# Optimization experiments

Measured on AMD Instinct MI355X. Metric: run time of the kernel, lower is better.

Reference implementation:

```python
import jax, jax.numpy as jnp
import numpy as np

N, E = 50000, 400000
IN, HID, LAT = 64, 64, 64


def _lin(key, fi, fo):
    return jax.random.normal(key, (fi, fo), jnp.float32) / np.sqrt(fi)


def setup_inputs() -> dict:
    key = jax.random.key(0)
    ks = jax.random.split(key, 24)
    inp = {
        'x': jax.random.normal(ks[0], (N, IN), jnp.float32),
        'edge_index': jax.random.randint(ks[1], (2, E), 0, N, dtype=jnp.int32),
        'batch': jnp.zeros((N,), jnp.int32),
    }
    # conv1: heads=1, out=HID, no residual
    inp.update(Wl1=_lin(ks[2], IN, HID), bl1=jnp.zeros(HID), Wr1=_lin(ks[3], IN, HID), br1=jnp.zeros(HID),
               att1=jax.random.normal(ks[4], (1, HID)) / np.sqrt(HID), bo1=jnp.zeros(HID))
    # conv2: heads=4, out=2*HID//4 per head (concat -> 2*HID), residual
    O2 = 2 * HID // 4
    inp.update(Wl2=_lin(ks[5], HID, 4 * O2), bl2=jnp.zeros(4 * O2), Wr2=_lin(ks[6], HID, 4 * O2), br2=jnp.zeros(4 * O2),
               att2=jax.random.normal(ks[7], (4, O2)) / np.sqrt(O2), bo2=jnp.zeros(4 * O2), Wres2=_lin(ks[8], HID, 4 * O2))
    # conv3: heads=4, out=HID per head (concat -> 4*HID), residual
    O3 = HID
    inp.update(Wl3=_lin(ks[9], 2 * HID, 4 * O3), bl3=jnp.zeros(4 * O3), Wr3=_lin(ks[10], 2 * HID, 4 * O3), br3=jnp.zeros(4 * O3),
               att3=jax.random.normal(ks[11], (4, O3)) / np.sqrt(O3), bo3=jnp.zeros(4 * O3), Wres3=_lin(ks[12], 2 * HID, 4 * O3))
    inp.update(ln1_g=jnp.ones(HID), ln1_b=jnp.zeros(HID), ln2_g=jnp.ones(2 * HID), ln2_b=jnp.zeros(2 * HID),
               ln3_g=jnp.ones(4 * HID), ln3_b=jnp.zeros(4 * HID))
    inp.update(enc_W=_lin(ks[13], 4 * HID, LAT), enc_b=jnp.zeros(LAT), rp_W=_lin(ks[14], IN, LAT), rp_b=jnp.zeros(LAT))
    inp.update(d1_W=_lin(ks[15], LAT, 2 * HID), d1_b=jnp.zeros(2 * HID), d2_W=_lin(ks[16], 2 * HID, HID), d2_b=jnp.zeros(HID),
               d3_W=_lin(ks[17], HID, IN), d3_b=jnp.zeros(IN))
    return inp


def _gatv2(x, src, tgt, Wl, bl, Wr, br, att, bo, heads, oc, Wres=None):
    # GATv2: e_ij = att . leaky_relu(Wr x_i + Wl x_j), softmax over in-neighbors of i,
    # out_i = sum_j alpha_ij * (Wl x_j); concat heads; optional linear residual.
    n = x.shape[0]
    xl = (x @ Wl + bl).reshape(n, heads, oc)  # source transform
    xr = (x @ Wr + br).reshape(n, heads, oc)  # target transform
    xj = xl[src]                              # [E, H, C] gathered source feats
    e = jnp.einsum('ehc,hc->eh', jax.nn.leaky_relu(xr[tgt] + xj, 0.2), att)
    m = jax.ops.segment_max(e, tgt, num_segments=n)          # stable segment softmax
    p = jnp.exp(e - m[tgt])
    alpha = p / jax.ops.segment_sum(p, tgt, num_segments=n)[tgt]
    out = jax.ops.segment_sum(alpha[:, :, None] * xj, tgt, num_segments=n).reshape(n, heads * oc)
    if Wres is not None:
        out = out + x @ Wres
    return out + bo


def _gnorm(x, g, b):
    # PyG LayerNorm(mode='graph') with batch=None: normalize over ALL nodes and features
    mu = jnp.mean(x)
    d = x - mu
    var = jnp.mean(d * d)
    return d * jax.lax.rsqrt(var + 1e-5) * g + b


def reference(x, edge_index, batch, Wl1, bl1, Wr1, br1, att1, bo1,
              Wl2, bl2, Wr2, br2, att2, bo2, Wres2,
              Wl3, bl3, Wr3, br3, att3, bo3, Wres3,
              ln1_g, ln1_b, ln2_g, ln2_b, ln3_g, ln3_b,
              enc_W, enc_b, rp_W, rp_b, d1_W, d1_b, d2_W, d2_b, d3_W, d3_b):
    n = x.shape[0]
    loop = jnp.arange(n, dtype=edge_index.dtype)  # add_self_loops=True (GATv2Conv default)
    src = jnp.concatenate([edge_index[0], loop])
    tgt = jnp.concatenate([edge_index[1], loop])
    h1 = jax.nn.relu(_gnorm(_gatv2(x, src, tgt, Wl1, bl1, Wr1, br1, att1, bo1, 1, HID), ln1_g, ln1_b))
    h2 = jax.nn.relu(_gnorm(_gatv2(h1, src, tgt, Wl2, bl2, Wr2, br2, att2, bo2, 4, 2 * HID // 4, Wres2), ln2_g, ln2_b))
    h3 = jax.nn.relu(_gnorm(_gatv2(h2, src, tgt, Wl3, bl3, Wr3, br3, att3, bo3, 4, HID, Wres3), ln3_g, ln3_b))
    z_nodes = jax.nn.relu(h3 @ enc_W + enc_b) + (x @ rp_W + rp_b)  # dropout inactive (eval)
    ones = jnp.ones((n, 1), z_nodes.dtype)
    z_graph = jax.ops.segment_sum(z_nodes, batch, num_segments=1) / jax.ops.segment_sum(ones, batch, num_segments=1)
    h = jax.nn.relu(z_nodes @ d1_W + d1_b)
    h = jax.nn.relu(h @ d2_W + d2_b)
    x_hat = h @ d3_W + d3_b
    return (z_nodes, x_hat, z_graph)
```

## Files before the change

### kernel.cpp

```cpp
#include <hip/hip_runtime.h>
#include <math.h>

typedef __attribute__((ext_vector_type(8))) short short8;
typedef __attribute__((ext_vector_type(4))) float f32x4;
typedef _Float16 h2 __attribute__((ext_vector_type(2)));

__device__ __forceinline__ unsigned short f2bf(float f) {
  union { float f; unsigned u; } c; c.f = f;
  unsigned r = c.u + 0x7fffu + ((c.u >> 16) & 1u);
  return (unsigned short)(r >> 16);
}
__device__ __forceinline__ float bf2f(unsigned short u) {
  union { unsigned u; float f; } c; c.u = ((unsigned)u) << 16;
  return c.f;
}
__device__ __forceinline__ void dot2(float& e, h2 a, h2 b) {
  asm("v_dot2_f32_f16 %0, %1, %2, %0" : "+v"(e) : "v"(a), "v"(b));
}

__global__ void zero_k(int* __restrict__ deg, int n, float* __restrict__ stats,
                       float* __restrict__ zg) {
  int i = blockIdx.x * 256 + threadIdx.x;
  if (i < n) deg[i] = 0;
  if (i < 768) stats[i] = 0.f;
  if (i < 64) zg[i] = 0.f;
}

__global__ void hist_k(const int* __restrict__ tgt, int* __restrict__ deg, int E) {
  int stride = gridDim.x * blockDim.x;
  for (int e = blockIdx.x * blockDim.x + threadIdx.x; e < E; e += stride)
    atomicAdd(&deg[tgt[e]], 1);
}

__global__ void scan1_k(const int* __restrict__ deg, int* __restrict__ bsum, int n) {
  __shared__ int sh[256];
  int idx = blockIdx.x * 256 + threadIdx.x;
  sh[threadIdx.x] = (idx < n) ? deg[idx] : 0;
  __syncthreads();
  for (int off = 128; off > 0; off >>= 1) {
    if (threadIdx.x < off) sh[threadIdx.x] += sh[threadIdx.x + off];
    __syncthreads();
  }
  if (threadIdx.x == 0) bsum[blockIdx.x] = sh[0];
}

__global__ void scan2_k(int* __restrict__ bsum, int nb) {
  __shared__ int sh[256];
  int t = threadIdx.x;
  int v = (t < nb) ? bsum[t] : 0;
  sh[t] = v; __syncthreads();
  for (int off = 1; off < 256; off <<= 1) {
    int add = (t >= off) ? sh[t - off] : 0;
    __syncthreads();
    sh[t] += add;
    __syncthreads();
  }
  if (t < nb) bsum[t] = sh[t] - v;
}

__global__ void scan3_k(const int* __restrict__ deg, const int* __restrict__ bsum,
                        int* __restrict__ starts, int* __restrict__ cursor, int n) {
  __shared__ int sh[256];
  int t = threadIdx.x;
  int idx = blockIdx.x * 256 + t;
  int v = (idx < n) ? deg[idx] : 0;
  sh[t] = v; __syncthreads();
  for (int off = 1; off < 256; off <<= 1) {
    int add = (t >= off) ? sh[t - off] : 0;
    __syncthreads();
    sh[t] += add;
    __syncthreads();
  }
  if (idx < n) {
    int ex = bsum[blockIdx.x] + sh[t] - v;
    starts[idx] = ex;
    cursor[idx] = ex;
  }
}

__global__ void scatter_k(const int* __restrict__ src, const int* __restrict__ tgt,
                          int* __restrict__ cursor, int* __restrict__ esrc, int E) {
  int stride = gridDim.x * blockDim.x;
  for (int e = blockIdx.x * blockDim.x + threadIdx.x; e < E; e += stride) {
    int p = atomicAdd(&cursor[tgt[e]], 1);
    esrc[p] = src[e];
  }
}

__global__ void cvt_k(const float* __restrict__ src, unsigned short* __restrict__ dst,
                      size_t n4) {
  size_t stride = (size_t)gridDim.x * blockDim.x;
  for (size_t i = (size_t)blockIdx.x * blockDim.x + threadIdx.x; i < n4; i += stride) {
    float4 v = reinterpret_cast<const float4*>(src)[i];
    ushort4 o;
    o.x = f2bf(v.x); o.y = f2bf(v.y); o.z = f2bf(v.z); o.w = f2bf(v.w);
    reinterpret_cast<ushort4*>(dst)[i] = o;
  }
}

struct WSeg { const float* W; unsigned short* T; int K; int F; int base; };
struct WPack { WSeg s[13]; int total; };
__global__ __launch_bounds__(256) void wconv_all_k(WPack p) {
  int idx = blockIdx.x * 256 + threadIdx.x;
  if (idx >= p.total) return;
  int si = 0;
#pragma unroll
  for (int i = 1; i < 13; ++i) si = (idx >= p.s[i].base) ? i : si;
  const WSeg sg = p.s[si];
  const int loc = idx - sg.base;
  const int k = loc / sg.F, f = loc - k * sg.F;
  sg.T[(size_t)f * sg.K + k] = f2bf(sg.W[loc]);
}

template <int K, int F, int SETS, int LNF, int OM0, int ACT1>
__global__ __launch_bounds__(256) void mg_k(
    const unsigned short* __restrict__ X, const float* __restrict__ bins,
    const float* __restrict__ lng, const float* __restrict__ lnb, float invNF,
    const unsigned short* __restrict__ WT0, const float* __restrict__ B0,
    const unsigned short* __restrict__ WT1, const float* __restrict__ B1,
    const unsigned short* __restrict__ WT2,
    _Float16* __restrict__ Y0, _Float16* __restrict__ Y1,
    unsigned short* __restrict__ Y2b, float* __restrict__ Y2f, int n) {
  constexpr int NK = K / 32;
  constexpr int TL = F / 64;
  constexpr int CPR = K / 8;
  __shared__ unsigned short As[64 * K];
  __shared__ float lnp[2];
  char* asb = (char*)As;
  const int tid = threadIdx.x;
  const int lane = tid & 63;
  const int wv = tid >> 6;
  const int r0 = blockIdx.x * 64;

  if (LNF) {
    if (tid < 64) {
      float s1 = bins[tid] + bins[tid + 64];
      float s2 = bins[tid + 128] + bins[tid + 192];
#pragma unroll
      for (int mm = 1; mm < 64; mm <<= 1) {
        s1 += __shfl_xor(s1, mm, 64);
        s2 += __shfl_xor(s2, mm, 64);
      }
      if (tid == 0) {
        const float mu = s1 * invNF;
        lnp[0] = mu;
        lnp[1] = rsqrtf(s2 * invNF - mu * mu + 1e-5f);
      }
    }
    __syncthreads();
  }
  const float mu = LNF ? lnp[0] : 0.f;
  const float rs = LNF ? lnp[1] : 0.f;

  for (int c = tid; c < 64 * CPR; c += 256) {
    const int row = c / CPR;
    const int k0 = (c - row * CPR) * 8;
    const int gr = r0 + row;
    short8 a = {0, 0, 0, 0, 0, 0, 0, 0};
    if (gr < n) {
      a = *reinterpret_cast<const short8*>(&X[(size_t)gr * K + k0]);
      if (LNF) {
        float g[8], bb[8];
        *(float4*)&g[0] = *(const float4*)&lng[k0];
        *(float4*)&g[4] = *(const float4*)&lng[k0 + 4];
        *(float4*)&bb[0] = *(const float4*)&lnb[k0];
        *(float4*)&bb[4] = *(const float4*)&lnb[k0 + 4];
#pragma unroll
        for (int q = 0; q < 8; ++q) {
          float f = bf2f((unsigned short)a[q]);
          f = fmaxf(fmaf(f - mu, rs * g[q], bb[q]), 0.f);
          a[q] = (short)f2bf(f);
        }
      }
    }
    const int boff = ((row * K + k0) * 2) ^ ((row & 7) << 4);
    *(short8*)(asb + boff) = a;
  }
  __syncthreads();

  const int rl = lane & 15;
  const int ks = lane >> 4;
#pragma unroll
  for (int set = 0; set < SETS; ++set) {
    const unsigned short* WT = (set == 0) ? WT0 : (set == 1) ? WT1 : WT2;
    f32x4 acc[4][TL];
#pragma unroll
    for (int rt = 0; rt < 4; ++rt)
#pragma unroll
      for (int t = 0; t < TL; ++t) acc[rt][t] = (f32x4){0.f, 0.f, 0.f, 0.f};
#pragma unroll
    for (int kk = 0; kk < NK; ++kk) {
      short8 bf[TL];
#pragma unroll
      for (int t = 0; t < TL; ++t)
        bf[t] = *reinterpret_cast<const short8*>(
            &WT[(size_t)((wv * TL + t) * 16 + rl) * K + kk * 32 + ks * 8]);
      short8 af[4];
#pragma unroll
      for (int rt = 0; rt < 4; ++rt) {
        const int row = rt * 16 + rl;
        const int boff = ((row * K + kk * 32 + ks * 8) * 2) ^ ((row & 7) << 4);
        af[rt] = *(const short8*)(asb + boff);
      }
#pragma unroll
      for (int rt = 0; rt < 4; ++rt)
#pragma unroll
        for (int t = 0; t < TL; ++t)
          acc[rt][t] =
              __builtin_amdgcn_mfma_f32_16x16x32_bf16(af[rt], bf[t], acc[rt][t], 0, 0, 0);
    }
#pragma unroll
    for (int rt = 0; rt < 4; ++rt) {
      const int rowd = r0 + rt * 16 + ks * 4;
#pragma unroll
      for (int t = 0; t < TL; ++t) {
        const int col = (wv * TL + t) * 16 + rl;
        const float bias = (set == 0) ? B0[col] : (set == 1) ? B1[col] : 0.f;
#pragma unroll
        for (int r = 0; r < 4; ++r) {
          const int gr = rowd + r;
          if (gr >= n) continue;
          float o = acc[rt][t][r] + bias;
          const size_t idx = (size_t)gr * F + col;
          if (set == 0) {
            if (ACT1) o = fmaxf(o, 0.f);
            if (OM0 == 0) Y0[idx] = (_Float16)o;
            else if (OM0 == 1) Y2b[idx] = f2bf(o);
            else Y2f[idx] = o;
          } else if (set == 1) {
            Y1[idx] = (_Float16)o;
          } else {
            Y2b[idx] = f2bf(o);
          }
        }
      }
    }
  }
}

__global__ __launch_bounds__(256) void enc_k(
    const unsigned short* __restrict__ h3, const float* __restrict__ bins,
    const float* __restrict__ lng, const float* __restrict__ lnb, float invNF,
    const unsigned short* __restrict__ WTe, const float* __restrict__ Be,
    const unsigned short* __restrict__ xb, const unsigned short* __restrict__ WTrp,
    const float* __restrict__ Brp, float* __restrict__ z,
    unsigned short* __restrict__ zb, int n) {
  constexpr int K1 = 256, K2 = 64, F = 64;
  __shared__ unsigned short As1[64 * K1];
  __shared__ unsigned short As2[64 * K2];
  __shared__ float lnp[2];
  char* a1b = (char*)As1;
  char* a2b = (char*)As2;
  const int tid = threadIdx.x;
  const int lane = tid & 63;
  const int wv = tid >> 6;
  const int r0 = blockIdx.x * 64;

  if (tid < 64) {
    float s1 = bins[tid] + bins[tid + 64];
    float s2 = bins[tid + 128] + bins[tid + 192];
#pragma unroll
    for (int mm = 1; mm < 64; mm <<= 1) {
      s1 += __shfl_xor(s1, mm, 64);
      s2 += __shfl_xor(s2, mm, 64);
    }
    if (tid == 0) {
      const float mu = s1 * invNF;
      lnp[0] = mu;
      lnp[1] = rsqrtf(s2 * invNF - mu * mu + 1e-5f);
    }
  }
  __syncthreads();
  const float mu = lnp[0], rs = lnp[1];

  for (int c = tid; c < 64 * (K1 / 8); c += 256) {
    const int row = c / (K1 / 8);
    const int k0 = (c - row * (K1 / 8)) * 8;
    const int gr = r0 + row;
    short8 a = {0, 0, 0, 0, 0, 0, 0, 0};
    if (gr < n) {
      a = *reinterpret_cast<const short8*>(&h3[(size_t)gr * K1 + k0]);
      float g[8], bb[8];
      *(float4*)&g[0] = *(const float4*)&lng[k0];
      *(float4*)&g[4] = *(const float4*)&lng[k0 + 4];
      *(float4*)&bb[0] = *(const float4*)&lnb[k0];
      *(float4*)&bb[4] = *(const float4*)&lnb[k0 + 4];
#pragma unroll
      for (int q = 0; q < 8; ++q) {
        float f = bf2f((unsigned short)a[q]);
        f = fmaxf(fmaf(f - mu, rs * g[q], bb[q]), 0.f);
        a[q] = (short)f2bf(f);
      }
    }
    const int boff = ((row * K1 + k0) * 2) ^ ((row & 7) << 4);
    *(short8*)(a1b + boff) = a;
  }
  for (int c = tid; c < 64 * (K2 / 8); c += 256) {
    const int row = c / (K2 / 8);
    const int k0 = (c - row * (K2 / 8)) * 8;
    const int gr = r0 + row;
    short8 a = {0, 0, 0, 0, 0, 0, 0, 0};
    if (gr < n) a = *reinterpret_cast<const short8*>(&xb[(size_t)gr * K2 + k0]);
    const int boff = ((row * K2 + k0) * 2) ^ ((row & 7) << 4);
    *(short8*)(a2b + boff) = a;
  }
  __syncthreads();

  const int rl = lane & 15;
  const int ks = lane >> 4;
  f32x4 a1[4], a2[4];
#pragma unroll
  for (int rt = 0; rt < 4; ++rt) {
    a1[rt] = (f32x4){0.f, 0.f, 0.f, 0.f};
    a2[rt] = (f32x4){0.f, 0.f, 0.f, 0.f};
  }
#pragma unroll
  for (int kk = 0; kk < K1 / 32; ++kk) {
    short8 bf = *reinterpret_cast<const short8*>(
        &WTe[(size_t)(wv * 16 + rl) * K1 + kk * 32 + ks * 8]);
#pragma unroll
    for (int rt = 0; rt < 4; ++rt) {
      const int row = rt * 16 + rl;
      const int boff = ((row * K1 + kk * 32 + ks * 8) * 2) ^ ((row & 7) << 4);
      short8 af = *(const short8*)(a1b + boff);
      a1[rt] = __builtin_amdgcn_mfma_f32_16x16x32_bf16(af, bf, a1[rt], 0, 0, 0);
    }
  }
#pragma unroll
  for (int kk = 0; kk < K2 / 32; ++kk) {
    short8 bf = *reinterpret_cast<const short8*>(
        &WTrp[(size_t)(wv * 16 + rl) * K2 + kk * 32 + ks * 8]);
#pragma unroll
    for (int rt = 0; rt < 4; ++rt) {
      const int row = rt * 16 + rl;
      const int boff = ((row * K2 + kk * 32 + ks * 8) * 2) ^ ((row & 7) << 4);
      short8 af = *(const short8*)(a2b + boff);
      a2[rt] = __builtin_amdgcn_mfma_f32_16x16x32_bf16(af, bf, a2[rt], 0, 0, 0);
    }
  }
  const int col = wv * 16 + rl;
  const float be = Be[col];
  const float brp = Brp[col];
#pragma unroll
  for (int rt = 0; rt < 4; ++rt) {
    const int rowd = r0 + rt * 16 + ks * 4;
#pragma unroll
    for (int r = 0; r < 4; ++r) {
      const int gr = rowd + r;
      if (gr >= n) continue;
      const float o = fmaxf(a1[rt][r] + be, 0.f) + a2[rt][r] + brp;
      const size_t idx = (size_t)gr * F + col;
      z[idx] = o;
      zb[idx] = f2bf(o);
    }
  }
}

template <int VEC> struct RawT;
template <> struct RawT<2> { using T = unsigned; };
template <> struct RawT<4> { using T = unsigned long long; };

template <int F, int H, int VEC, int HAS_RES>
__global__ __launch_bounds__(256) void agg_k(
    const _Float16* __restrict__ xl, const _Float16* __restrict__ xr,
    const float* __restrict__ att, const float* __restrict__ bo,
    const int* __restrict__ starts, const int* __restrict__ deg,
    const int* __restrict__ esrc, unsigned short* __restrict__ out,
    float* __restrict__ bins, int n) {
  constexpr int G = 64 / H;
  constexpr int NP = VEC / 2;
  using RT = typename RawT<VEC>::T;
  union PU { RT r; h2 h[NP]; _Float16 e[VEC]; };
  const h2 HC = {(_Float16)0.2f, (_Float16)0.2f};
  const h2 HZ = {(_Float16)0.f, (_Float16)0.f};
  const int lane = threadIdx.x & 63;
  const int wv = threadIdx.x >> 6;
  const int node = blockIdx.x * 4 + wv;
  const bool active = node < n;
  const int nl = active ? node : 0;
  float s1w = 0.f, s2w = 0.f;

  const RT* xlr = (const RT*)xl;
  PU xru; xru.r = ((const RT*)xr)[(size_t)nl * 64 + lane];
  h2 attp[NP];
  float bov[VEC];
  PU resu; resu.r = 0;
#pragma unroll
  for (int pp = 0; pp < NP; ++pp) {
    attp[pp][0] = (_Float16)att[lane * VEC + pp * 2];
    attp[pp][1] = (_Float16)att[lane * VEC + pp * 2 + 1];
  }
#pragma unroll
  for (int q = 0; q < VEC; ++q) bov[q] = bo[lane * VEC + q];
  unsigned short resb[VEC];
  if (HAS_RES) {
#pragma unroll
    for (int q = 0; q < VEC; ++q) resb[q] = out[(size_t)nl * F + lane * VEC + q];
  }
  int st = 0, cnt = 0;
  if (active) { st = starts[node]; cnt = deg[node]; }
  const int total = active ? cnt + 1 : 0;
  auto LD = [&](int i) -> RT {
    const int j = (i < cnt) ? esrc[st + i] : nl;
    return xlr[(size_t)j * 64 + lane];
  };
  float m = -1e30f, s = 0.f, acc[VEC];
#pragma unroll
  for (int q = 0; q < VEC; ++q) acc[q] = 0.f;

  RT q0 = LD(0), q1 = LD(1), q2 = LD(2), q3 = LD(3);
  for (int it = 0; it < total; it += 2) {
    const RT f0 = LD(it + 4), f1 = LD(it + 5);
    PU x0, x1; x0.r = q0; x1.r = q1;
    float e0 = 0.f, e1 = 0.f;
#pragma unroll
    for (int pp = 0; pp < NP; ++pp) {
      h2 t0 = xru.h[pp] + x0.h[pp];
      h2 t1 = xru.h[pp] + x1.h[pp];
      h2 lk0 = __builtin_elementwise_fma(__builtin_elementwise_min(t0, HZ), HC,
                                         __builtin_elementwise_max(t0, HZ));
      h2 lk1 = __builtin_elementwise_fma(__builtin_elementwise_min(t1, HZ), HC,
                                         __builtin_elementwise_max(t1, HZ));
      dot2(e0, lk0, attp[pp]);
      dot2(e1, lk1, attp[pp]);
    }
#pragma unroll
    for (int mask = 1; mask < G; mask <<= 1) {
      e0 += __shfl_xor(e0, mask, 64);
      e1 += __shfl_xor(e1, mask, 64);
    }
    if (it + 1 >= total) e1 = -1e30f;
    const float eM = fmaxf(e0, e1);
    if (eM - m > 8.f) {
      const float sc = __expf(m - eM);
      s *= sc;
#pragma unroll
      for (int q = 0; q < VEC; ++q) acc[q] *= sc;
      m = eM;
    }
    const float p0 = __expf(e0 - m);
    const float p1 = __expf(e1 - m);
    s += p0 + p1;
#pragma unroll
    for (int q = 0; q < VEC; ++q)
      acc[q] = fmaf(p0, (float)x0.e[q], fmaf(p1, (float)x1.e[q], acc[q]));
    q0 = q2; q1 = q3; q2 = f0; q3 = f1;
  }
  if (active) {
    const float inv = 1.f / s;
#pragma unroll
    for (int q = 0; q < VEC; ++q) {
      float o = acc[q] * inv + bov[q];
      if (HAS_RES) o += bf2f(resb[q]);
      out[(size_t)node * F + lane * VEC + q] = f2bf(o);
      s1w += o;
      s2w += o * o;
    }
  }
#pragma unroll
  for (int mask = 1; mask < 64; mask <<= 1) {
    s1w += __shfl_xor(s1w, mask, 64);
    s2w += __shfl_xor(s2w, mask, 64);
  }
  __shared__ float sh[8];
  if (lane == 0) { sh[wv] = s1w; sh[4 + wv] = s2w; }
  __syncthreads();
  if (threadIdx.x == 0) {
    const int bin = blockIdx.x & 127;
    atomicAdd(&bins[bin], sh[0] + sh[1] + sh[2] + sh[3]);
    atomicAdd(&bins[128 + bin], sh[4] + sh[5] + sh[6] + sh[7]);
  }
}

__global__ __launch_bounds__(256) void agg1_k(
    const _Float16* __restrict__ xl, const _Float16* __restrict__ xr,
    const float* __restrict__ att, const float* __restrict__ bo,
    const int* __restrict__ starts, const int* __restrict__ deg,
    const int* __restrict__ esrc, unsigned short* __restrict__ out,
    float* __restrict__ bins, int n) {
  union PU { unsigned r; h2 h; _Float16 e[2]; };
  const h2 HC = {(_Float16)0.2f, (_Float16)0.2f};
  const h2 HZ = {(_Float16)0.f, (_Float16)0.f};
  const int lane = threadIdx.x & 63;
  const int wv = threadIdx.x >> 6;
  const int l32 = lane & 31;
  const int node = blockIdx.x * 8 + wv * 2 + (lane >> 5);
  const bool active = node < n;
  const int nl = active ? node : 0;
  float s1w = 0.f, s2w = 0.f;

  const unsigned* xlr = (const unsigned*)xl;
  PU xru; xru.r = ((const unsigned*)xr)[(size_t)nl * 32 + l32];
  h2 attp = {(_Float16)att[l32 * 2], (_Float16)att[l32 * 2 + 1]};
  const float bo0 = bo[l32 * 2], bo1 = bo[l32 * 2 + 1];
  int st = 0, cnt = 0;
  if (active) { st = starts[node]; cnt = deg[node]; }
  const int total = active ? cnt + 1 : 0;
  const int mt = max(total, __shfl_xor(total, 32, 64));
  auto LD = [&](int i) -> unsigned {
    const int j = (i < cnt) ? esrc[st + i] : nl;
    return xlr[(size_t)j * 32 + l32];
  };
  float m = -1e30f, s = 0.f, a0 = 0.f, a1 = 0.f;
  unsigned q0 = LD(0), q1 = LD(1), q2 = LD(2), q3 = LD(3);
  for (int it = 0; it < mt; it += 2) {
    const unsigned f0 = LD(it + 4), f1 = LD(it + 5);
    PU x0, x1; x0.r = q0; x1.r = q1;
    float e0 = 0.f, e1 = 0.f;
    {
      h2 t0 = xru.h + x0.h;
      h2 t1 = xru.h + x1.h;
      h2 lk0 = __builtin_elementwise_fma(__builtin_elementwise_min(t0, HZ), HC,
                                         __builtin_elementwise_max(t0, HZ));
      h2 lk1 = __builtin_elementwise_fma(__builtin_elementwise_min(t1, HZ), HC,
                                         __builtin_elementwise_max(t1, HZ));
      dot2(e0, lk0, attp);
      dot2(e1, lk1, attp);
    }
#pragma unroll
    for (int mask = 1; mask < 32; mask <<= 1) {
      e0 += __shfl_xor(e0, mask, 64);
      e1 += __shfl_xor(e1, mask, 64);
    }
    if (it >= total) e0 = -1e30f;
    if (it + 1 >= total) e1 = -1e30f;
    const float eM = fmaxf(e0, e1);
    if (eM - m > 8.f && eM > -1e29f) {
      const float sc = __expf(m - eM);
      s *= sc; a0 *= sc; a1 *= sc;
      m = eM;
    }
    const float p0 = __expf(e0 - m);
    const float p1 = __expf(e1 - m);
    s += p0 + p1;
    a0 = fmaf(p0, (float)x0.e[0], fmaf(p1, (float)x1.e[0], a0));
    a1 = fmaf(p0, (float)x0.e[1], fmaf(p1, (float)x1.e[1], a1));
    q0 = q2; q1 = q3; q2 = f0; q3 = f1;
  }
  if (active) {
    const float inv = 1.f / s;
    const float o0 = a0 * inv + bo0;
    const float o1 = a1 * inv + bo1;
    out[(size_t)node * 64 + l32 * 2] = f2bf(o0);
    out[(size_t)node * 64 + l32 * 2 + 1] = f2bf(o1);
    s1w = o0 + o1;
    s2w = o0 * o0 + o1 * o1;
  }
#pragma unroll
  for (int mask = 1; mask < 64; mask <<= 1) {
    s1w += __shfl_xor(s1w, mask, 64);
    s2w += __shfl_xor(s2w, mask, 64);
  }
  __shared__ float sh[8];
  if (lane == 0) { sh[wv] = s1w; sh[4 + wv] = s2w; }
  __syncthreads();
  if (threadIdx.x == 0) {
    const int bin = blockIdx.x & 127;
    atomicAdd(&bins[bin], sh[0] + sh[1] + sh[2] + sh[3]);
    atomicAdd(&bins[128 + bin], sh[4] + sh[5] + sh[6] + sh[7]);
  }
}

__global__ void colmean_k(const float* __restrict__ z, float* __restrict__ outv,
                          int n, float inv) {
  __shared__ float sh[256];
  int col = threadIdx.x & 63;
  int w = threadIdx.x >> 6;
  float s = 0.f;
  for (int r = blockIdx.x * 4 + w; r < n; r += gridDim.x * 4)
    s += z[(size_t)r * 64 + col];
  sh[threadIdx.x] = s;
  __syncthreads();
  if (threadIdx.x < 64) {
    float t = sh[threadIdx.x] + sh[threadIdx.x + 64] + sh[threadIdx.x + 128] +
              sh[threadIdx.x + 192];
    atomicAdd(&outv[col], t * inv);
  }
}

extern "C" void kernel_launch(void* const* d_in, const int* in_sizes, int n_in,
                              void* d_out, int out_size, void* d_ws, size_t ws_size,
                              hipStream_t stream) {
  const float* x = (const float*)d_in[0];
  const int* ei = (const int*)d_in[1];
  const float *Wl1 = (const float*)d_in[3], *bl1 = (const float*)d_in[4];
  const float *Wr1 = (const float*)d_in[5], *br1 = (const float*)d_in[6];
  const float *att1 = (const float*)d_in[7], *bo1 = (const float*)d_in[8];
  const float *Wl2 = (const float*)d_in[9], *bl2 = (const float*)d_in[10];
  const float *Wr2 = (const float*)d_in[11], *br2 = (const float*)d_in[12];
  const float *att2 = (const float*)d_in[13], *bo2 = (const float*)d_in[14];
  const float *Wres2 = (const float*)d_in[15];
  const float *Wl3 = (const float*)d_in[16], *bl3 = (const float*)d_in[17];
  const float *Wr3 = (const float*)d_in[18], *br3 = (const float*)d_in[19];
  const float *att3 = (const float*)d_in[20], *bo3 = (const float*)d_in[21];
  const float *Wres3 = (const float*)d_in[22];
  const float *ln1g = (const float*)d_in[23], *ln1b = (const float*)d_in[24];
  const float *ln2g = (const float*)d_in[25], *ln2b = (const float*)d_in[26];
  const float *ln3g = (const float*)d_in[27], *ln3b = (const float*)d_in[28];
  const float *encW = (const float*)d_in[29], *encb = (const float*)d_in[30];
  const float *rpW = (const float*)d_in[31], *rpb = (const float*)d_in[32];
  const float *d1W = (const float*)d_in[33], *d1b = (const float*)d_in[34];
  const float *d2W = (const float*)d_in[35], *d2b = (const float*)d_in[36];
  const float *d3W = (const float*)d_in[37], *d3b = (const float*)d_in[38];

  const int N = in_sizes[0] / 64;
  const int E = in_sizes[1] / 2;
  const int* esrc_in = ei;
  const int* etgt_in = ei + E;

  char* cur = (char*)d_ws;
  auto take = [&](size_t bytes) {
    char* p = cur;
    cur += (bytes + 15) & ~(size_t)15;
    return p;
  };
  unsigned short* bufCb = (unsigned short*)take((size_t)N * 256 * 2);
  unsigned short* bufDb = (unsigned short*)take((size_t)N * 128 * 2);
  _Float16* Ab = (_Float16*)take((size_t)N * 256 * 2);
  _Float16* Bb = (_Float16*)take((size_t)N * 256 * 2);
  unsigned short* Cb = (unsigned short*)take((size_t)N * 256 * 2);
  unsigned short* Db = (unsigned short*)take((size_t)N * 128 * 2);
  unsigned short* xb = (unsigned short*)take((size_t)N * 64 * 2);
  float* stats = (float*)take(768 * 4);
  int* deg = (int*)take((size_t)N * 4);
  int* starts = (int*)take((size_t)N * 4);
  int* cursor = (int*)take((size_t)N * 4);
  int* bsum = (int*)take(1024);
  int* esrc = (int*)take((size_t)E * 4);
  auto wt = [&](int K, int F) { return (unsigned short*)take((size_t)K * F * 2); };
  unsigned short *Tl1 = wt(64, 64), *Tr1 = wt(64, 64);
  unsigned short *Tl2 = wt(64, 128), *Tr2 = wt(64, 128), *Tres2 = wt(64, 128);
  unsigned short *Tl3 = wt(128, 256), *Tr3 = wt(128, 256), *Tres3 = wt(128, 256);
  unsigned short *Tenc = wt(256, 64), *Trp = wt(64, 64);
  unsigned short *Td1 = wt(64, 128), *Td2 = wt(128, 64), *Td3 = wt(64, 64);
  if ((size_t)(cur - (char*)d_ws) > ws_size) return;

  float* z = (float*)d_out;
  float* xhat = z + (size_t)N * 64;
  float* zg = xhat + (size_t)N * 64;

  zero_k<<<(N + 255) / 256, 256, 0, stream>>>(deg, N, stats, zg);

  {
    WPack p;
    const float* Ws[13] = {Wl1, Wr1, Wl2, Wr2, Wres2, Wl3, Wr3, Wres3,
                           encW, rpW, d1W, d2W, d3W};
    unsigned short* Ts[13] = {Tl1, Tr1, Tl2, Tr2, Tres2, Tl3, Tr3, Tres3,
                              Tenc, Trp, Td1, Td2, Td3};
    const int Ks[13] = {64, 64, 64, 64, 64, 128, 128, 128, 256, 64, 64, 128, 64};
    const int Fs[13] = {64, 64, 128, 128, 128, 256, 256, 256, 64, 64, 128, 64, 64};
    int base = 0;
    for (int i = 0; i < 13; ++i) {
      p.s[i] = {Ws[i], Ts[i], Ks[i], Fs[i], base};
      base += Ks[i] * Fs[i];
    }
    p.total = base;
    wconv_all_k<<<(base + 255) / 256, 256, 0, stream>>>(p);
  }
  cvt_k<<<1024, 256, 0, stream>>>(x, xb, (size_t)N * 16);

  const int nb = (N + 255) / 256;
  hist_k<<<512, 256, 0, stream>>>(etgt_in, deg, E);
  scan1_k<<<nb, 256, 0, stream>>>(deg, bsum, N);
  scan2_k<<<1, 256, 0, stream>>>(bsum, nb);
  scan3_k<<<nb, 256, 0, stream>>>(deg, bsum, starts, cursor, N);
  scatter_k<<<512, 256, 0, stream>>>(esrc_in, etgt_in, cursor, esrc, E);

  const int gblk = (N + 63) / 64;
  const int ablk = (N + 3) / 4;
  const float* nullf = nullptr;
  _Float16* nullh = nullptr;
  unsigned short* nullb = nullptr;
  float* nully = nullptr;

  mg_k<64, 64, 2, 0, 0, 0><<<gblk, 256, 0, stream>>>(
      xb, nullf, nullf, nullf, 0.f, Tl1, bl1, Tr1, br1, nullb, Ab, Bb, nullb, nully, N);
  agg1_k<<<(N + 7) / 8, 256, 0, stream>>>(Ab, Bb, att1, bo1, starts, deg, esrc, bufCb,
                                          stats + 0, N);
  mg_k<64, 128, 3, 1, 0, 0><<<gblk, 256, 0, stream>>>(
      bufCb, stats + 0, ln1g, ln1b, 1.f / ((float)N * 64.f), Tl2, bl2, Tr2, br2, Tres2,
      Ab, Bb, bufDb, nully, N);
  agg_k<128, 4, 2, 1><<<ablk, 256, 0, stream>>>(Ab, Bb, att2, bo2, starts, deg, esrc,
                                                bufDb, stats + 256, N);
  mg_k<128, 256, 3, 1, 0, 0><<<gblk, 256, 0, stream>>>(
      bufDb, stats + 256, ln2g, ln2b, 1.f / ((float)N * 128.f), Tl3, bl3, Tr3, br3,
      Tres3, Ab, Bb, bufCb, nully, N);
  agg_k<256, 4, 4, 1><<<ablk, 256, 0, stream>>>(Ab, Bb, att3, bo3, starts, deg, esrc,
                                                bufCb, stats + 512, N);
  enc_k<<<gblk, 256, 0, stream>>>(bufCb, stats + 512, ln3g, ln3b,
                                  1.f / ((float)N * 256.f), Tenc, encb, xb, Trp, rpb, z,
                                  xb, N);
  colmean_k<<<256, 256, 0, stream>>>(z, zg, N, 1.f / (float)N);

  mg_k<64, 128, 1, 0, 1, 1><<<gblk, 256, 0, stream>>>(
      xb, nullf, nullf, nullf, 0.f, Td1, d1b, nullb, nullf, nullb, nullh, nullh, Db,
      nully, N);
  mg_k<128, 64, 1, 0, 1, 1><<<gblk, 256, 0, stream>>>(
      Db, nullf, nullf, nullf, 0.f, Td2, d2b, nullb, nullf, nullb, nullh, nullh, Cb,
      nully, N);
  mg_k<64, 64, 1, 0, 2, 0><<<gblk, 256, 0, stream>>>(
      Cb, nullf, nullf, nullf, 0.f, Td3, d3b, nullb, nullf, nullb, nullh, nullh, nullb,
      xhat, N);
}
```

Before: 506.9 us.

## Fuse prep kernels, unify aggregation template, fuse encoder with decoder MLP

Merges the weight conversion, input bf16 cast and zeroing kernels into one prep launch. Replaces the separate aggregation kernels with a single template in which two lane groups process alternating edges, with fp16 accumulation, a tighter rescale threshold and vectorised stores. Fuses the encoder, the three decoder layers and a partial column mean into one kernel that keeps intermediates in shared memory, followed by a tiny finalisation kernel. This removes launches and the HBM round trips for the decoder intermediates, at the cost of fp16 accumulation precision in the softmax sums.

```diff
diff --git a/kernel.cpp b/kernel.cpp
--- a/kernel.cpp
+++ b/kernel.cpp
@@ -16,14 +16,6 @@
 }
 __device__ __forceinline__ void dot2(float& e, h2 a, h2 b) {
   asm("v_dot2_f32_f16 %0, %1, %2, %0" : "+v"(e) : "v"(a), "v"(b));
-}
-
-__global__ void zero_k(int* __restrict__ deg, int n, float* __restrict__ stats,
-                       float* __restrict__ zg) {
-  int i = blockIdx.x * 256 + threadIdx.x;
-  if (i < n) deg[i] = 0;
-  if (i < 768) stats[i] = 0.f;
-  if (i < 64) zg[i] = 0.f;
 }
 
 __global__ void hist_k(const int* __restrict__ tgt, int* __restrict__ deg, int E) {
@@ -87,32 +79,42 @@
   }
 }
 
-__global__ void cvt_k(const float* __restrict__ src, unsigned short* __restrict__ dst,
-                      size_t n4) {
-  size_t stride = (size_t)gridDim.x * blockDim.x;
-  for (size_t i = (size_t)blockIdx.x * blockDim.x + threadIdx.x; i < n4; i += stride) {
-    float4 v = reinterpret_cast<const float4*>(src)[i];
-    ushort4 o;
-    o.x = f2bf(v.x); o.y = f2bf(v.y); o.z = f2bf(v.z); o.w = f2bf(v.w);
-    reinterpret_cast<ushort4*>(dst)[i] = o;
-  }
-}
-
 struct WSeg { const float* W; unsigned short* T; int K; int F; int base; };
 struct WPack { WSeg s[13]; int total; };
-__global__ __launch_bounds__(256) void wconv_all_k(WPack p) {
-  int idx = blockIdx.x * 256 + threadIdx.x;
-  if (idx >= p.total) return;
-  int si = 0;
-#pragma unroll
-  for (int i = 1; i < 13; ++i) si = (idx >= p.s[i].base) ? i : si;
-  const WSeg sg = p.s[si];
-  const int loc = idx - sg.base;
-  const int k = loc / sg.F, f = loc - k * sg.F;
-  sg.T[(size_t)f * sg.K + k] = f2bf(sg.W[loc]);
-}
-
-template <int K, int F, int SETS, int LNF, int OM0, int ACT1>
+__global__ __launch_bounds__(256) void prep_k(WPack p, int WB, const float* __restrict__ x,
+                                              unsigned short* __restrict__ xb, size_t n4,
+                                              int CB, int* __restrict__ deg, int n,
+                                              float* __restrict__ stats,
+                                              float* __restrict__ zgb) {
+  const int bid = blockIdx.x;
+  const int tid = threadIdx.x;
+  if (bid < WB) {
+    int idx = bid * 256 + tid;
+    if (idx >= p.total) return;
+    int si = 0;
+#pragma unroll
+    for (int i = 1; i < 13; ++i) si = (idx >= p.s[i].base) ? i : si;
+    const WSeg sg = p.s[si];
+    const int loc = idx - sg.base;
+    const int k = loc / sg.F, f = loc - k * sg.F;
+    sg.T[(size_t)f * sg.K + k] = f2bf(sg.W[loc]);
+  } else if (bid < WB + CB) {
+    size_t stride = (size_t)CB * 256;
+    for (size_t i = (size_t)(bid - WB) * 256 + tid; i < n4; i += stride) {
+      float4 v = reinterpret_cast<const float4*>(x)[i];
+      ushort4 o;
+      o.x = f2bf(v.x); o.y = f2bf(v.y); o.z = f2bf(v.z); o.w = f2bf(v.w);
+      reinterpret_cast<ushort4*>(xb)[i] = o;
+    }
+  } else {
+    int zi = (bid - WB - CB) * 256 + tid;
+    if (zi < n) deg[zi] = 0;
+    if (zi < 768) stats[zi] = 0.f;
+    if (zi < 1024) zgb[zi] = 0.f;
+  }
+}
+
+template <int K, int F, int SETS, int LNF>
 __global__ __launch_bounds__(256) void mg_k(
     const unsigned short* __restrict__ X, const float* __restrict__ bins,
     const float* __restrict__ lng, const float* __restrict__ lnb, float invNF,
@@ -120,7 +122,7 @@
     const unsigned short* __restrict__ WT1, const float* __restrict__ B1,
     const unsigned short* __restrict__ WT2,
     _Float16* __restrict__ Y0, _Float16* __restrict__ Y1,
-    unsigned short* __restrict__ Y2b, float* __restrict__ Y2f, int n) {
+    unsigned short* __restrict__ Y2b, int n) {
   constexpr int NK = K / 32;
   constexpr int TL = F / 64;
   constexpr int CPR = K / 8;
@@ -222,239 +224,166 @@
           if (gr >= n) continue;
           float o = acc[rt][t][r] + bias;
           const size_t idx = (size_t)gr * F + col;
-          if (set == 0) {
-            if (ACT1) o = fmaxf(o, 0.f);
-            if (OM0 == 0) Y0[idx] = (_Float16)o;
-            else if (OM0 == 1) Y2b[idx] = f2bf(o);
-            else Y2f[idx] = o;
-          } else if (set == 1) {
-            Y1[idx] = (_Float16)o;
-          } else {
-            Y2b[idx] = f2bf(o);
-          }
+          if (set == 0) Y0[idx] = (_Float16)o;
+          else if (set == 1) Y1[idx] = (_Float16)o;
+          else Y2b[idx] = f2bf(o);
         }
       }
     }
   }
 }
 
-__global__ __launch_bounds__(256) void enc_k(
-    const unsigned short* __restrict__ h3, const float* __restrict__ bins,
-    const float* __restrict__ lng, const float* __restrict__ lnb, float invNF,
-    const unsigned short* __restrict__ WTe, const float* __restrict__ Be,
-    const unsigned short* __restrict__ xb, const unsigned short* __restrict__ WTrp,
-    const float* __restrict__ Brp, float* __restrict__ z,
-    unsigned short* __restrict__ zb, int n) {
-  constexpr int K1 = 256, K2 = 64, F = 64;
-  __shared__ unsigned short As1[64 * K1];
-  __shared__ unsigned short As2[64 * K2];
-  __shared__ float lnp[2];
-  char* a1b = (char*)As1;
-  char* a2b = (char*)As2;
-  const int tid = threadIdx.x;
-  const int lane = tid & 63;
-  const int wv = tid >> 6;
-  const int r0 = blockIdx.x * 64;
-
-  if (tid < 64) {
-    float s1 = bins[tid] + bins[tid + 64];
-    float s2 = bins[tid + 128] + bins[tid + 192];
-#pragma unroll
-    for (int mm = 1; mm < 64; mm <<= 1) {
-      s1 += __shfl_xor(s1, mm, 64);
-      s2 += __shfl_xor(s2, mm, 64);
-    }
-    if (tid == 0) {
-      const float mu = s1 * invNF;
-      lnp[0] = mu;
-      lnp[1] = rsqrtf(s2 * invNF - mu * mu + 1e-5f);
-    }
-  }
-  __syncthreads();
-  const float mu = lnp[0], rs = lnp[1];
-
-  for (int c = tid; c < 64 * (K1 / 8); c += 256) {
-    const int row = c / (K1 / 8);
-    const int k0 = (c - row * (K1 / 8)) * 8;
-    const int gr = r0 + row;
-    short8 a = {0, 0, 0, 0, 0, 0, 0, 0};
-    if (gr < n) {
-      a = *reinterpret_cast<const short8*>(&h3[(size_t)gr * K1 + k0]);
-      float g[8], bb[8];
-      *(float4*)&g[0] = *(const float4*)&lng[k0];
-      *(float4*)&g[4] = *(const float4*)&lng[k0 + 4];
-      *(float4*)&bb[0] = *(const float4*)&lnb[k0];
-      *(float4*)&bb[4] = *(const float4*)&lnb[k0 + 4];
-#pragma unroll
-      for (int q = 0; q < 8; ++q) {
-        float f = bf2f((unsigned short)a[q]);
-        f = fmaxf(fmaf(f - mu, rs * g[q], bb[q]), 0.f);
-        a[q] = (short)f2bf(f);
-      }
-    }
-    const int boff = ((row * K1 + k0) * 2) ^ ((row & 7) << 4);
-    *(short8*)(a1b + boff) = a;
-  }
-  for (int c = tid; c < 64 * (K2 / 8); c += 256) {
-    const int row = c / (K2 / 8);
-    const int k0 = (c - row * (K2 / 8)) * 8;
-    const int gr = r0 + row;
-    short8 a = {0, 0, 0, 0, 0, 0, 0, 0};
-    if (gr < n) a = *reinterpret_cast<const short8*>(&xb[(size_t)gr * K2 + k0]);
-    const int boff = ((row * K2 + k0) * 2) ^ ((row & 7) << 4);
-    *(short8*)(a2b + boff) = a;
-  }
-  __syncthreads();
-
-  const int rl = lane & 15;
-  const int ks = lane >> 4;
-  f32x4 a1[4], a2[4];
-#pragma unroll
-  for (int rt = 0; rt < 4; ++rt) {
-    a1[rt] = (f32x4){0.f, 0.f, 0.f, 0.f};
-    a2[rt] = (f32x4){0.f, 0.f, 0.f, 0.f};
-  }
-#pragma unroll
-  for (int kk = 0; kk < K1 / 32; ++kk) {
-    short8 bf = *reinterpret_cast<const short8*>(
-        &WTe[(size_t)(wv * 16 + rl) * K1 + kk * 32 + ks * 8]);
-#pragma unroll
-    for (int rt = 0; rt < 4; ++rt) {
-      const int row = rt * 16 + rl;
-      const int boff = ((row * K1 + kk * 32 + ks * 8) * 2) ^ ((row & 7) << 4);
-      short8 af = *(const short8*)(a1b + boff);
-      a1[rt] = __builtin_amdgcn_mfma_f32_16x16x32_bf16(af, bf, a1[rt], 0, 0, 0);
-    }
-  }
-#pragma unroll
-  for (int kk = 0; kk < K2 / 32; ++kk) {
-    short8 bf = *reinterpret_cast<const short8*>(
-        &WTrp[(size_t)(wv * 16 + rl) * K2 + kk * 32 + ks * 8]);
-#pragma unroll
-    for (int rt = 0; rt < 4; ++rt) {
-      const int row = rt * 16 + rl;
-      const int boff = ((row * K2 + kk * 32 + ks * 8) * 2) ^ ((row & 7) << 4);
-      short8 af = *(const short8*)(a2b + boff);
-      a2[rt] = __builtin_amdgcn_mfma_f32_16x16x32_bf16(af, bf, a2[rt], 0, 0, 0);
-    }
-  }
-  const int col = wv * 16 + rl;
-  const float be = Be[col];
-  const float brp = Brp[col];
-#pragma unroll
-  for (int rt = 0; rt < 4; ++rt) {
-    const int rowd = r0 + rt * 16 + ks * 4;
-#pragma unroll
-    for (int r = 0; r < 4; ++r) {
-      const int gr = rowd + r;
-      if (gr >= n) continue;
-      const float o = fmaxf(a1[rt][r] + be, 0.f) + a2[rt][r] + brp;
-      const size_t idx = (size_t)gr * F + col;
-      z[idx] = o;
-      zb[idx] = f2bf(o);
-    }
-  }
-}
-
-template <int VEC> struct RawT;
-template <> struct RawT<2> { using T = unsigned; };
-template <> struct RawT<4> { using T = unsigned long long; };
-
-template <int F, int H, int VEC, int HAS_RES>
-__global__ __launch_bounds__(256) void agg_k(
+template <int F, int H, int NPW, int HAS_RES>
+__global__ __launch_bounds__(256) void agg_t(
     const _Float16* __restrict__ xl, const _Float16* __restrict__ xr,
     const float* __restrict__ att, const float* __restrict__ bo,
     const int* __restrict__ starts, const int* __restrict__ deg,
     const int* __restrict__ esrc, unsigned short* __restrict__ out,
     float* __restrict__ bins, int n) {
-  constexpr int G = 64 / H;
+  constexpr int LPN = 64 / NPW;
+  constexpr int LPE = LPN / 2;
+  constexpr int VEC = F / LPE;
   constexpr int NP = VEC / 2;
-  using RT = typename RawT<VEC>::T;
-  union PU { RT r; h2 h[NP]; _Float16 e[VEC]; };
+  constexpr int RED = LPE / H;
+  union PU { unsigned u[NP]; h2 h[NP]; _Float16 e[VEC]; };
   const h2 HC = {(_Float16)0.2f, (_Float16)0.2f};
   const h2 HZ = {(_Float16)0.f, (_Float16)0.f};
   const int lane = threadIdx.x & 63;
   const int wv = threadIdx.x >> 6;
-  const int node = blockIdx.x * 4 + wv;
+  const int le = lane & (LPN - 1);
+  const int sub = le / LPE;
+  const int l_e = le & (LPE - 1);
+  const int node = blockIdx.x * 4 * NPW + wv * NPW + ((NPW == 2) ? (lane >> 5) : 0);
   const bool active = node < n;
   const int nl = active ? node : 0;
-  float s1w = 0.f, s2w = 0.f;
-
-  const RT* xlr = (const RT*)xl;
-  PU xru; xru.r = ((const RT*)xr)[(size_t)nl * 64 + lane];
+  const int ch0 = l_e * VEC;
+
+  auto loadrow = [&](int j, PU& r) {
+    const char* p = (const char*)xl + ((size_t)j * F + ch0) * 2;
+    if constexpr (VEC == 8) {
+      uint4 v = *(const uint4*)p;
+      r.u[0] = v.x; r.u[1] = v.y; r.u[2] = v.z; r.u[3] = v.w;
+    } else {
+      uint2 v = *(const uint2*)p;
+      r.u[0] = v.x; r.u[1] = v.y;
+    }
+  };
+
+  PU xru;
+  loadrow(0, xru);
+  {
+    const char* p = (const char*)xr + ((size_t)nl * F + ch0) * 2;
+    if constexpr (VEC == 8) {
+      uint4 v = *(const uint4*)p;
+      xru.u[0] = v.x; xru.u[1] = v.y; xru.u[2] = v.z; xru.u[3] = v.w;
+    } else {
+      uint2 v = *(const uint2*)p;
+      xru.u[0] = v.x; xru.u[1] = v.y;
+    }
+  }
   h2 attp[NP];
   float bov[VEC];
-  PU resu; resu.r = 0;
+  unsigned short resb[VEC];
 #pragma unroll
   for (int pp = 0; pp < NP; ++pp) {
-    attp[pp][0] = (_Float16)att[lane * VEC + pp * 2];
-    attp[pp][1] = (_Float16)att[lane * VEC + pp * 2 + 1];
-  }
-#pragma unroll
-  for (int q = 0; q < VEC; ++q) bov[q] = bo[lane * VEC + q];
-  unsigned short resb[VEC];
-  if (HAS_RES) {
-#pragma unroll
-    for (int q = 0; q < VEC; ++q) resb[q] = out[(size_t)nl * F + lane * VEC + q];
+    attp[pp][0] = (_Float16)att[ch0 + pp * 2];
+    attp[pp][1] = (_Float16)att[ch0 + pp * 2 + 1];
+  }
+#pragma unroll
+  for (int q = 0; q < VEC; ++q) {
+    bov[q] = bo[ch0 + q];
+    if (HAS_RES) resb[q] = out[(size_t)nl * F + ch0 + q];
   }
   int st = 0, cnt = 0;
   if (active) { st = starts[node]; cnt = deg[node]; }
   const int total = active ? cnt + 1 : 0;
-  auto LD = [&](int i) -> RT {
-    const int j = (i < cnt) ? esrc[st + i] : nl;
-    return xlr[(size_t)j * 64 + lane];
+  int mt = total;
+  if constexpr (NPW == 2) {
+    int ot = __shfl_xor(total, 32, 64);
+    mt = max(total, ot);
+  }
+  auto getj = [&](int idx) -> int {
+    int j = nl;
+    if (idx < cnt) j = esrc[st + idx];
+    return j;
   };
-  float m = -1e30f, s = 0.f, acc[VEC];
-#pragma unroll
-  for (int q = 0; q < VEC; ++q) acc[q] = 0.f;
-
-  RT q0 = LD(0), q1 = LD(1), q2 = LD(2), q3 = LD(3);
-  for (int it = 0; it < total; it += 2) {
-    const RT f0 = LD(it + 4), f1 = LD(it + 5);
-    PU x0, x1; x0.r = q0; x1.r = q1;
-    float e0 = 0.f, e1 = 0.f;
+
+  float m = -1e30f, s = 0.f;
+  PU acc;
+#pragma unroll
+  for (int pp = 0; pp < NP; ++pp) acc.h[pp] = HZ;
+
+  PU r0, r1;
+  loadrow(getj(0 + sub), r0);
+  loadrow(getj(2 + sub), r1);
+  for (int it = 0; it < mt; it += 2) {
+    PU rn;
+    loadrow(getj(it + 4 + sub), rn);
+    float e = 0.f;
 #pragma unroll
     for (int pp = 0; pp < NP; ++pp) {
-      h2 t0 = xru.h[pp] + x0.h[pp];
-      h2 t1 = xru.h[pp] + x1.h[pp];
-      h2 lk0 = __builtin_elementwise_fma(__builtin_elementwise_min(t0, HZ), HC,
-                                         __builtin_elementwise_max(t0, HZ));
-      h2 lk1 = __builtin_elementwise_fma(__builtin_elementwise_min(t1, HZ), HC,
-                                         __builtin_elementwise_max(t1, HZ));
-      dot2(e0, lk0, attp[pp]);
-      dot2(e1, lk1, attp[pp]);
-    }
-#pragma unroll
-    for (int mask = 1; mask < G; mask <<= 1) {
-      e0 += __shfl_xor(e0, mask, 64);
-      e1 += __shfl_xor(e1, mask, 64);
-    }
-    if (it + 1 >= total) e1 = -1e30f;
-    const float eM = fmaxf(e0, e1);
-    if (eM - m > 8.f) {
+      h2 t = xru.h[pp] + r0.h[pp];
+      h2 lk = __builtin_elementwise_fma(__builtin_elementwise_min(t, HZ), HC,
+                                        __builtin_elementwise_max(t, HZ));
+      dot2(e, lk, attp[pp]);
+    }
+#pragma unroll
+    for (int mask = 1; mask < RED; mask <<= 1) e += __shfl_xor(e, mask, 64);
+    if (it + sub >= total) e = -1e30f;
+    const float eo = __shfl_xor(e, LPE, 64);
+    const float eM = fmaxf(e, eo);
+    if (eM - m > 4.f) {
       const float sc = __expf(m - eM);
       s *= sc;
-#pragma unroll
-      for (int q = 0; q < VEC; ++q) acc[q] *= sc;
+      const _Float16 sch = (_Float16)sc;
+      const h2 sv = {sch, sch};
+#pragma unroll
+      for (int pp = 0; pp < NP; ++pp) acc.h[pp] *= sv;
       m = eM;
     }
-    const float p0 = __expf(e0 - m);
-    const float p1 = __expf(e1 - m);
-    s += p0 + p1;
-#pragma unroll
-    for (int q = 0; q < VEC; ++q)
-      acc[q] = fmaf(p0, (float)x0.e[q], fmaf(p1, (float)x1.e[q], acc[q]));
-    q0 = q2; q1 = q3; q2 = f0; q3 = f1;
-  }
-  if (active) {
-    const float inv = 1.f / s;
+    const float p = __expf(e - m);
+    s += p;
+    const _Float16 ph = (_Float16)p;
+    const h2 pv = {ph, ph};
+#pragma unroll
+    for (int pp = 0; pp < NP; ++pp)
+      acc.h[pp] = __builtin_elementwise_fma(pv, r0.h[pp], acc.h[pp]);
+    r0 = r1;
+    r1 = rn;
+  }
+  const float stot = s + __shfl_xor(s, LPE, 64);
+  PU at;
+#pragma unroll
+  for (int pp = 0; pp < NP; ++pp) {
+    PU tmp;
+    tmp.u[0] = __shfl_xor(acc.u[pp], LPE, 64);
+    at.h[pp] = acc.h[pp] + tmp.h[0];
+  }
+  float s1w = 0.f, s2w = 0.f;
+  if (active && sub == 0) {
+    const float inv = 1.f / stot;
+    unsigned short ov[VEC];
 #pragma unroll
     for (int q = 0; q < VEC; ++q) {
-      float o = acc[q] * inv + bov[q];
+      float o = (float)at.e[q] * inv + bov[q];
       if (HAS_RES) o += bf2f(resb[q]);
-      out[(size_t)node * F + lane * VEC + q] = f2bf(o);
+      ov[q] = f2bf(o);
       s1w += o;
       s2w += o * o;
+    }
+    char* op = (char*)out + ((size_t)node * F + ch0) * 2;
+    if constexpr (VEC == 8) {
+      uint4 v;
+      v.x = (unsigned)ov[0] | ((unsigned)ov[1] << 16);
+      v.y = (unsigned)ov[2] | ((unsigned)ov[3] << 16);
+      v.z = (unsigned)ov[4] | ((unsigned)ov[5] << 16);
+      v.w = (unsigned)ov[6] | ((unsigned)ov[7] << 16);
+      *(uint4*)op = v;
+    } else {
+      uint2 v;
+      v.x = (unsigned)ov[0] | ((unsigned)ov[1] << 16);
+      v.y = (unsigned)ov[2] | ((unsigned)ov[3] << 16);
+      *(uint2*)op = v;
     }
   }
 #pragma unroll
@@ -472,110 +401,245 @@
   }
 }
 
-__global__ __launch_bounds__(256) void agg1_k(
-    const _Float16* __restrict__ xl, const _Float16* __restrict__ xr,
-    const float* __restrict__ att, const float* __restrict__ bo,
-    const int* __restrict__ starts, const int* __restrict__ deg,
-    const int* __restrict__ esrc, unsigned short* __restrict__ out,
-    float* __restrict__ bins, int n) {
-  union PU { unsigned r; h2 h; _Float16 e[2]; };
-  const h2 HC = {(_Float16)0.2f, (_Float16)0.2f};
-  const h2 HZ = {(_Float16)0.f, (_Float16)0.f};
-  const int lane = threadIdx.x & 63;
-  const int wv = threadIdx.x >> 6;
-  const int l32 = lane & 31;
-  const int node = blockIdx.x * 8 + wv * 2 + (lane >> 5);
-  const bool active = node < n;
-  const int nl = active ? node : 0;
-  float s1w = 0.f, s2w = 0.f;
-
-  const unsigned* xlr = (const unsigned*)xl;
-  PU xru; xru.r = ((const unsigned*)xr)[(size_t)nl * 32 + l32];
-  h2 attp = {(_Float16)att[l32 * 2], (_Float16)att[l32 * 2 + 1]};
-  const float bo0 = bo[l32 * 2], bo1 = bo[l32 * 2 + 1];
-  int st = 0, cnt = 0;
-  if (active) { st = starts[node]; cnt = deg[node]; }
-  const int total = active ? cnt + 1 : 0;
-  const int mt = max(total, __shfl_xor(total, 32, 64));
-  auto LD = [&](int i) -> unsigned {
-    const int j = (i < cnt) ? esrc[st + i] : nl;
-    return xlr[(size_t)j * 32 + l32];
-  };
-  float m = -1e30f, s = 0.f, a0 = 0.f, a1 = 0.f;
-  unsigned q0 = LD(0), q1 = LD(1), q2 = LD(2), q3 = LD(3);
-  for (int it = 0; it < mt; it += 2) {
-    const unsigned f0 = LD(it + 4), f1 = LD(it + 5);
-    PU x0, x1; x0.r = q0; x1.r = q1;
-    float e0 = 0.f, e1 = 0.f;
-    {
-      h2 t0 = xru.h + x0.h;
-      h2 t1 = xru.h + x1.h;
-      h2 lk0 = __builtin_elementwise_fma(__builtin_elementwise_min(t0, HZ), HC,
-                                         __builtin_elementwise_max(t0, HZ));
-      h2 lk1 = __builtin_elementwise_fma(__builtin_elementwise_min(t1, HZ), HC,
-                                         __builtin_elementwise_max(t1, HZ));
-      dot2(e0, lk0, attp);
-      dot2(e1, lk1, attp);
-    }
-#pragma unroll
-    for (int mask = 1; mask < 32; mask <<= 1) {
-      e0 += __shfl_xor(e0, mask, 64);
-      e1 += __shfl_xor(e1, mask, 64);
-    }
-    if (it >= total) e0 = -1e30f;
-    if (it + 1 >= total) e1 = -1e30f;
-    const float eM = fmaxf(e0, e1);
-    if (eM - m > 8.f && eM > -1e29f) {
-      const float sc = __expf(m - eM);
-      s *= sc; a0 *= sc; a1 *= sc;
-      m = eM;
-    }
-    const float p0 = __expf(e0 - m);
-    const float p1 = __expf(e1 - m);
-    s += p0 + p1;
-    a0 = fmaf(p0, (float)x0.e[0], fmaf(p1, (float)x1.e[0], a0));
-    a1 = fmaf(p0, (float)x0.e[1], fmaf(p1, (float)x1.e[1], a1));
-    q0 = q2; q1 = q3; q2 = f0; q3 = f1;
-  }
-  if (active) {
-    const float inv = 1.f / s;
-    const float o0 = a0 * inv + bo0;
-    const float o1 = a1 * inv + bo1;
-    out[(size_t)node * 64 + l32 * 2] = f2bf(o0);
-    out[(size_t)node * 64 + l32 * 2 + 1] = f2bf(o1);
-    s1w = o0 + o1;
-    s2w = o0 * o0 + o1 * o1;
-  }
-#pragma unroll
-  for (int mask = 1; mask < 64; mask <<= 1) {
-    s1w += __shfl_xor(s1w, mask, 64);
-    s2w += __shfl_xor(s2w, mask, 64);
-  }
-  __shared__ float sh[8];
-  if (lane == 0) { sh[wv] = s1w; sh[4 + wv] = s2w; }
+__global__ __launch_bounds__(256) void encdec_k(
+    const unsigned short* __restrict__ h3, const float* __restrict__ bins,
+    const float* __restrict__ lng, const float* __restrict__ lnb, float invNF,
+    const unsigned short* __restrict__ WTe, const float* __restrict__ Be,
+    const unsigned short* __restrict__ xb, const unsigned short* __restrict__ WTrp,
+    const float* __restrict__ Brp, const unsigned short* __restrict__ Td1,
+    const float* __restrict__ d1b, const unsigned short* __restrict__ Td2,
+    const float* __restrict__ d2b, const unsigned short* __restrict__ Td3,
+    const float* __restrict__ d3b, float* __restrict__ z, float* __restrict__ xhat,
+    float* __restrict__ zgb, int n) {
+  __shared__ char smem[49152];
+  char* a1b = smem;
+  char* a2b = smem + 32768;
+  char* zsb = smem + 40960;
+  __shared__ float lnp[2];
+  const int tid = threadIdx.x;
+  const int lane = tid & 63;
+  const int wv = tid >> 6;
+  const int rl = lane & 15;
+  const int ks = lane >> 4;
+  const int r0 = blockIdx.x * 64;
+
+  if (tid < 64) {
+    float s1 = bins[tid] + bins[tid + 64];
+    float s2 = bins[tid + 128] + bins[tid + 192];
+#pragma unroll
+    for (int mm = 1; mm < 64; mm <<= 1) {
+      s1 += __shfl_xor(s1, mm, 64);
+      s2 += __shfl_xor(s2, mm, 64);
+    }
+    if (tid == 0) {
+      const float mu = s1 * invNF;
+      lnp[0] = mu;
+      lnp[1] = rsqrtf(s2 * invNF - mu * mu + 1e-5f);
+    }
+  }
   __syncthreads();
-  if (threadIdx.x == 0) {
-    const int bin = blockIdx.x & 127;
-    atomicAdd(&bins[bin], sh[0] + sh[1] + sh[2] + sh[3]);
-    atomicAdd(&bins[128 + bin], sh[4] + sh[5] + sh[6] + sh[7]);
-  }
-}
-
-__global__ void colmean_k(const float* __restrict__ z, float* __restrict__ outv,
-                          int n, float inv) {
-  __shared__ float sh[256];
-  int col = threadIdx.x & 63;
-  int w = threadIdx.x >> 6;
+  const float mu = lnp[0], rs = lnp[1];
+
+  for (int c = tid; c < 64 * 32; c += 256) {
+    const int row = c / 32;
+    const int k0 = (c - row * 32) * 8;
+    const int gr = r0 + row;
+    short8 a = {0, 0, 0, 0, 0, 0, 0, 0};
+    if (gr < n) {
+      a = *reinterpret_cast<const short8*>(&h3[(size_t)gr * 256 + k0]);
+      float g[8], bb[8];
+      *(float4*)&g[0] = *(const float4*)&lng[k0];
+      *(float4*)&g[4] = *(const float4*)&lng[k0 + 4];
+      *(float4*)&bb[0] = *(const float4*)&lnb[k0];
+      *(float4*)&bb[4] = *(const float4*)&lnb[k0 + 4];
+#pragma unroll
+      for (int q = 0; q < 8; ++q) {
+        float f = bf2f((unsigned short)a[q]);
+        f = fmaxf(fmaf(f - mu, rs * g[q], bb[q]), 0.f);
+        a[q] = (short)f2bf(f);
+      }
+    }
+    const int boff = ((row * 256 + k0) * 2) ^ ((row & 7) << 4);
+    *(short8*)(a1b + boff) = a;
+  }
+  for (int c = tid; c < 64 * 8; c += 256) {
+    const int row = c / 8;
+    const int k0 = (c - row * 8) * 8;
+    const int gr = r0 + row;
+    short8 a = {0, 0, 0, 0, 0, 0, 0, 0};
+    if (gr < n) a = *reinterpret_cast<const short8*>(&xb[(size_t)gr * 64 + k0]);
+    const int boff = ((row * 64 + k0) * 2) ^ ((row & 7) << 4);
+    *(short8*)(a2b + boff) = a;
+  }
+  __syncthreads();
+
+  {
+    f32x4 a1[4], a2[4];
+#pragma unroll
+    for (int rt = 0; rt < 4; ++rt) {
+      a1[rt] = (f32x4){0.f, 0.f, 0.f, 0.f};
+      a2[rt] = (f32x4){0.f, 0.f, 0.f, 0.f};
+    }
+#pragma unroll
+    for (int kk = 0; kk < 8; ++kk) {
+      short8 bfr = *reinterpret_cast<const short8*>(
+          &WTe[(size_t)(wv * 16 + rl) * 256 + kk * 32 + ks * 8]);
+#pragma unroll
+      for (int rt = 0; rt < 4; ++rt) {
+        const int row = rt * 16 + rl;
+        const int boff = ((row * 256 + kk * 32 + ks * 8) * 2) ^ ((row & 7) << 4);
+        short8 af = *(const short8*)(a1b + boff);
+        a1[rt] = __builtin_amdgcn_mfma_f32_16x16x32_bf16(af, bfr, a1[rt], 0, 0, 0);
+      }
+    }
+#pragma unroll
+    for (int kk = 0; kk < 2; ++kk) {
+      short8 bfr = *reinterpret_cast<const short8*>(
+          &WTrp[(size_t)(wv * 16 + rl) * 64 + kk * 32 + ks * 8]);
+#pragma unroll
+      for (int rt = 0; rt < 4; ++rt) {
+        const int row = rt * 16 + rl;
+        const int boff = ((row * 64 + kk * 32 + ks * 8) * 2) ^ ((row & 7) << 4);
+        short8 af = *(const short8*)(a2b + boff);
+        a2[rt] = __builtin_amdgcn_mfma_f32_16x16x32_bf16(af, bfr, a2[rt], 0, 0, 0);
+      }
+    }
+    const int col = wv * 16 + rl;
+    const float be = Be[col];
+    const float brp = Brp[col];
+    float colpart = 0.f;
+#pragma unroll
+    for (int rt = 0; rt < 4; ++rt) {
+#pragma unroll
+      for (int r = 0; r < 4; ++r) {
+        const int lrow = rt * 16 + ks * 4 + r;
+        const int gr = r0 + lrow;
+        float o = fmaxf(a1[rt][r] + be, 0.f) + a2[rt][r] + brp;
+        if (gr < n) {
+          z[(size_t)gr * 64 + col] = o;
+          colpart += o;
+        } else {
+          o = 0.f;
+        }
+        const int boff = ((lrow * 64 + col) * 2) ^ ((lrow & 7) << 4);
+        *(unsigned short*)(zsb + boff) = f2bf(o);
+      }
+    }
+    colpart += __shfl_xor(colpart, 16, 64);
+    colpart += __shfl_xor(colpart, 32, 64);
+    if (lane < 16) atomicAdd(&zgb[(blockIdx.x & 15) * 64 + col], colpart);
+  }
+  __syncthreads();
+
+  {
+    f32x4 acc[4][2];
+#pragma unroll
+    for (int rt = 0; rt < 4; ++rt) {
+      acc[rt][0] = (f32x4){0.f, 0.f, 0.f, 0.f};
+      acc[rt][1] = (f32x4){0.f, 0.f, 0.f, 0.f};
+    }
+#pragma unroll
+    for (int kk = 0; kk < 2; ++kk) {
+      short8 bfr[2];
+#pragma unroll
+      for (int t = 0; t < 2; ++t)
+        bfr[t] = *reinterpret_cast<const short8*>(
+            &Td1[(size_t)((wv * 2 + t) * 16 + rl) * 64 + kk * 32 + ks * 8]);
+#pragma unroll
+      for (int rt = 0; rt < 4; ++rt) {
+        const int row = rt * 16 + rl;
+        const int boff = ((row * 64 + kk * 32 + ks * 8) * 2) ^ ((row & 7) << 4);
+        short8 af = *(const short8*)(zsb + boff);
+#pragma unroll
+        for (int t = 0; t < 2; ++t)
+          acc[rt][t] = __builtin_amdgcn_mfma_f32_16x16x32_bf16(af, bfr[t], acc[rt][t], 0, 0, 0);
+      }
+    }
+#pragma unroll
+    for (int rt = 0; rt < 4; ++rt) {
+#pragma unroll
+      for (int t = 0; t < 2; ++t) {
+        const int col = (wv * 2 + t) * 16 + rl;
+        const float bias = d1b[col];
+#pragma unroll
+        for (int r = 0; r < 4; ++r) {
+          const int row = rt * 16 + ks * 4 + r;
+          const float o = fmaxf(acc[rt][t][r] + bias, 0.f);
+          const int boff = ((row * 128 + col) * 2) ^ ((row & 7) << 4);
+          *(unsigned short*)(a1b + boff) = f2bf(o);
+        }
+      }
+    }
+  }
+  __syncthreads();
+
+  {
+    f32x4 acc[4];
+#pragma unroll
+    for (int rt = 0; rt < 4; ++rt) acc[rt] = (f32x4){0.f, 0.f, 0.f, 0.f};
+#pragma unroll
+    for (int kk = 0; kk < 4; ++kk) {
+      short8 bfr = *reinterpret_cast<const short8*>(
+          &Td2[(size_t)(wv * 16 + rl) * 128 + kk * 32 + ks * 8]);
+#pragma unroll
+      for (int rt = 0; rt < 4; ++rt) {
+        const int row = rt * 16 + rl;
+        const int boff = ((row * 128 + kk * 32 + ks * 8) * 2) ^ ((row & 7) << 4);
+        short8 af = *(const short8*)(a1b + boff);
+        acc[rt] = __builtin_amdgcn_mfma_f32_16x16x32_bf16(af, bfr, acc[rt], 0, 0, 0);
+      }
+    }
+    const int col = wv * 16 + rl;
+    const float bias = d2b[col];
+#pragma unroll
+    for (int rt = 0; rt < 4; ++rt) {
+#pragma unroll
+      for (int r = 0; r < 4; ++r) {
+        const int row = rt * 16 + ks * 4 + r;
+        const float o = fmaxf(acc[rt][r] + bias, 0.f);
+        const int boff = ((row * 64 + col) * 2) ^ ((row & 7) << 4);
+        *(unsigned short*)(a2b + boff) = f2bf(o);
+      }
+    }
+  }
+  __syncthreads();
+
+  {
+    f32x4 acc[4];
+#pragma unroll
+    for (int rt = 0; rt < 4; ++rt) acc[rt] = (f32x4){0.f, 0.f, 0.f, 0.f};
+#pragma unroll
+    for (int kk = 0; kk < 2; ++kk) {
+      short8 bfr = *reinterpret_cast<const short8*>(
+          &Td3[(size_t)(wv * 16 + rl) * 64 + kk * 32 + ks * 8]);
+#pragma unroll
+      for (int rt = 0; rt < 4; ++rt) {
+        const int row = rt * 16 + rl;
+        const int boff = ((row * 64 + kk * 32 + ks * 8) * 2) ^ ((row & 7) << 4);
+        short8 af = *(const short8*)(a2b + boff);
+        acc[rt] = __builtin_amdgcn_mfma_f32_16x16x32_bf16(af, bfr, acc[rt], 0, 0, 0);
+      }
+    }
+    const int col = wv * 16 + rl;
+    const float bias = d3b[col];
+#pragma unroll
+    for (int rt = 0; rt < 4; ++rt) {
+#pragma unroll
+      for (int r = 0; r < 4; ++r) {
+        const int gr = r0 + rt * 16 + ks * 4 + r;
+        if (gr < n) xhat[(size_t)gr * 64 + col] = acc[rt][r] + bias;
+      }
+    }
+  }
+}
+
+__global__ void colfin_k(const float* __restrict__ zgb, float* __restrict__ zg,
+                         float invN) {
+  const int c = threadIdx.x;
   float s = 0.f;
-  for (int r = blockIdx.x * 4 + w; r < n; r += gridDim.x * 4)
-    s += z[(size_t)r * 64 + col];
-  sh[threadIdx.x] = s;
-  __syncthreads();
-  if (threadIdx.x < 64) {
-    float t = sh[threadIdx.x] + sh[threadIdx.x + 64] + sh[threadIdx.x + 128] +
-              sh[threadIdx.x + 192];
-    atomicAdd(&outv[col], t * inv);
-  }
+#pragma unroll
+  for (int b = 0; b < 16; ++b) s += zgb[b * 64 + c];
+  zg[c] = s * invN;
 }
 
 extern "C" void kernel_launch(void* const* d_in, const int* in_sizes, int n_in,
@@ -618,10 +682,9 @@
   unsigned short* bufDb = (unsigned short*)take((size_t)N * 128 * 2);
   _Float16* Ab = (_Float16*)take((size_t)N * 256 * 2);
   _Float16* Bb = (_Float16*)take((size_t)N * 256 * 2);
-  unsigned short* Cb = (unsigned short*)take((size_t)N * 256 * 2);
-  unsigned short* Db = (unsigned short*)take((size_t)N * 128 * 2);
   unsigned short* xb = (unsigned short*)take((size_t)N * 64 * 2);
   float* stats = (float*)take(768 * 4);
+  float* zgb = (float*)take(1024 * 4);
   int* deg = (int*)take((size_t)N * 4);
   int* starts = (int*)take((size_t)N * 4);
   int* cursor = (int*)take((size_t)N * 4);
@@ -639,8 +702,6 @@
   float* xhat = z + (size_t)N * 64;
   float* zg = xhat + (size_t)N * 64;
 
-  zero_k<<<(N + 255) / 256, 256, 0, stream>>>(deg, N, stats, zg);
-
   {
     WPack p;
     const float* Ws[13] = {Wl1, Wr1, Wl2, Wr2, Wres2, Wl3, Wr3, Wres3,
@@ -655,9 +716,12 @@
       base += Ks[i] * Fs[i];
     }
     p.total = base;
-    wconv_all_k<<<(base + 255) / 256, 256, 0, stream>>>(p);
-  }
-  cvt_k<<<1024, 256, 0, stream>>>(x, xb, (size_t)N * 16);
+    const int WB = (base + 255) / 256;
+    const int CB = 512;
+    const int ZB = (N + 255) / 256;
+    prep_k<<<WB + CB + ZB, 256, 0, stream>>>(p, WB, x, xb, (size_t)N * 16, CB, deg, N,
+                                             stats, zgb);
+  }
 
   const int nb = (N + 255) / 256;
   hist_k<<<512, 256, 0, stream>>>(etgt_in, deg, E);
@@ -667,38 +731,25 @@
   scatter_k<<<512, 256, 0, stream>>>(esrc_in, etgt_in, cursor, esrc, E);
 
   const int gblk = (N + 63) / 64;
-  const int ablk = (N + 3) / 4;
   const float* nullf = nullptr;
-  _Float16* nullh = nullptr;
   unsigned short* nullb = nullptr;
-  float* nully = nullptr;
-
-  mg_k<64, 64, 2, 0, 0, 0><<<gblk, 256, 0, stream>>>(
-      xb, nullf, nullf, nullf, 0.f, Tl1, bl1, Tr1, br1, nullb, Ab, Bb, nullb, nully, N);
-  agg1_k<<<(N + 7) / 8, 256, 0, stream>>>(Ab, Bb, att1, bo1, starts, deg, esrc, bufCb,
-                                          stats + 0, N);
-  mg_k<64, 128, 3, 1, 0, 0><<<gblk, 256, 0, stream>>>(
+
+  mg_k<64, 64, 2, 0><<<gblk, 256, 0, stream>>>(xb, nullf, nullf, nullf, 0.f, Tl1, bl1,
+                                               Tr1, br1, nullb, Ab, Bb, nullb, N);
+  agg_t<64, 1, 2, 0><<<(N + 7) / 8, 256, 0, stream>>>(Ab, Bb, att1, bo1, starts, deg,
+                                                      esrc, bufCb, stats + 0, N);
+  mg_k<64, 128, 3, 1><<<gblk, 256, 0, stream>>>(
       bufCb, stats + 0, ln1g, ln1b, 1.f / ((float)N * 64.f), Tl2, bl2, Tr2, br2, Tres2,
-      Ab, Bb, bufDb, nully, N);
-  agg_k<128, 4, 2, 1><<<ablk, 256, 0, stream>>>(Ab, Bb, att2, bo2, starts, deg, esrc,
-                                                bufDb, stats + 256, N);
-  mg_k<128, 256, 3, 1, 0, 0><<<gblk, 256, 0, stream>>>(
+      Ab, Bb, bufDb, N);
+  agg_t<128, 4, 1, 1><<<(N + 3) / 4, 256, 0, stream>>>(Ab, Bb, att2, bo2, starts, deg,
+                                                       esrc, bufDb, stats + 256, N);
+  mg_k<128, 256, 3, 1><<<gblk, 256, 0, stream>>>(
       bufDb, stats + 256, ln2g, ln2b, 1.f / ((float)N * 128.f), Tl3, bl3, Tr3, br3,
-      Tres3, Ab, Bb, bufCb, nully, N);
-  agg_k<256, 4, 4, 1><<<ablk, 256, 0, stream>>>(Ab, Bb, att3, bo3, starts, deg, esrc,
-                                                bufCb, stats + 512, N);
-  enc_k<<<gblk, 256, 0, stream>>>(bufCb, stats + 512, ln3g, ln3b,
-                                  1.f / ((float)N * 256.f), Tenc, encb, xb, Trp, rpb, z,
-                                  xb, N);
-  colmean_k<<<256, 256, 0, stream>>>(z, zg, N, 1.f / (float)N);
-
-  mg_k<64, 128, 1, 0, 1, 1><<<gblk, 256, 0, stream>>>(
-      xb, nullf, nullf, nullf, 0.f, Td1, d1b, nullb, nullf, nullb, nullh, nullh, Db,
-      nully, N);
-  mg_k<128, 64, 1, 0, 1, 1><<<gblk, 256, 0, stream>>>(
-      Db, nullf, nullf, nullf, 0.f, Td2, d2b, nullb, nullf, nullb, nullh, nullh, Cb,
-      nully, N);
-  mg_k<64, 64, 1, 0, 2, 0><<<gblk, 256, 0, stream>>>(
-      Cb, nullf, nullf, nullf, 0.f, Td3, d3b, nullb, nullf, nullb, nullh, nullh, nullb,
-      xhat, N);
-}
+      Tres3, Ab, Bb, bufCb, N);
+  agg_t<256, 4, 1, 1><<<(N + 3) / 4, 256, 0, stream>>>(Ab, Bb, att3, bo3, starts, deg,
+                                                       esrc, bufCb, stats + 512, N);
+  encdec_k<<<gblk, 256, 0, stream>>>(bufCb, stats + 512, ln3g, ln3b,
+                                     1.f / ((float)N * 256.f), Tenc, encb, xb, Trp, rpb,
+                                     Td1, d1b, Td2, d2b, Td3, d3b, z, xhat, zgb, N);
+  colfin_k<<<1, 64, 0, stream>>>(zgb, zg, 1.f / (float)N);
+}
```

Result: faster. 448.7 us (-11.5%).
